# Performance work log

Measured on AMD Instinct MI355X. Metric: run time of the kernel, lower is better.

The kernel has to match this reference:

```python
import jax, jax.numpy as jnp
import numpy as np
from jax import lax

BIN_SIZE = 16.0
SIGMA = 2.0
THRESHOLD = 0.3
MIN_VOTES = 50.0
ACC = 24  # static accumulator extent per dim; provably >= max bin span for these inputs
BIG = 1_000_000


def setup_inputs() -> dict:
    key = jax.random.key(0)
    k1, k2 = jax.random.split(key)
    offsets = jax.random.normal(k1, (4, 2, 256, 256), dtype=jnp.float32)
    foreground_mask = jax.random.randint(k2, (4, 256, 256), 0, 2).astype(bool)
    return {"offsets": offsets, "foreground_mask": foreground_mask}


def hough_labels(offsets, foreground_mask):
    B, S = offsets.shape[:2]
    H, W = offsets.shape[2:]
    N = H * W

    # coordinate grid: channel 0 = x (last spatial dim), channel 1 = y (reversed meshgrid)
    ys, xs = jnp.meshgrid(jnp.arange(H, dtype=jnp.float32),
                          jnp.arange(W, dtype=jnp.float32), indexing='ij')
    coords = jnp.stack([xs, ys], axis=0)                      # [2, H, W]

    votes = coords[None] + offsets                            # [B, 2, H, W]
    bins = jnp.round(votes / BIN_SIZE).astype(jnp.int32).reshape(B, S, N)  # [B, 2, N]
    fg = foreground_mask.reshape(B, N)                        # [B, N]

    # per-batch min bin over foreground pixels -> shift to non-negative indices
    bin_min = jnp.min(jnp.where(fg[:, None, :], bins, BIG), axis=2)        # [B, 2]
    shifted = bins - bin_min[:, :, None]                                   # [B, 2, N]
    bin_max = jnp.max(jnp.where(fg[:, None, :], shifted, -1), axis=2) + 1  # [B, 2]

    # scatter-add vote counts into a static [ACC, ACC] accumulator per batch
    s0 = jnp.clip(shifted[:, 0], 0, ACC - 1)
    s1 = jnp.clip(shifted[:, 1], 0, ACC - 1)
    w = fg.astype(jnp.float32)
    bidx = jnp.broadcast_to(jnp.arange(B)[:, None], (B, N))
    acc = jnp.zeros((B, ACC, ACC), jnp.float32).at[bidx, s0, s1].add(w)

    # mean-filter smoothing (k = int(3*sigma)*2+1), zero padding, same shape
    k = int(3 * SIGMA) * 2 + 1
    kernel = jnp.ones((1, 1, k, k), jnp.float32) / float(k * k)
    sm = lax.conv_general_dilated(acc[:, None], kernel, (1, 1),
                                  [(k // 2, k // 2)] * 2)[:, 0]            # [B, ACC, ACC]

    # zero out cells beyond the tight (data-dependent) torch accumulator extent
    i = jnp.arange(ACC)
    valid = (i[None, :, None] < bin_max[:, 0, None, None]) & \
            (i[None, None, :] < bin_max[:, 1, None, None])
    sm = jnp.where(valid, sm, 0.0)

    # peak detection: relative threshold vs min_votes floor
    thr = jnp.maximum(sm.max(axis=(1, 2)) * THRESHOLD, MIN_VOTES)          # [B]
    peaks = (sm >= thr[:, None, None]).reshape(B, ACC * ACC)               # [B, C]
    # 1-based row-major rank of each peak cell (matches torch.nonzero ordering)
    ranks = jnp.cumsum(peaks.astype(jnp.int32), axis=1)                    # [B, C]

    # nearest-peak assignment (squared L2 preserves cdist argmin)
    c0, c1 = jnp.meshgrid(i, i, indexing='ij')
    cells = jnp.stack([c0.ravel(), c1.ravel()], axis=-1).astype(jnp.float32)  # [C, 2]
    fb = shifted.transpose(0, 2, 1).astype(jnp.float32)                    # [B, N, 2]
    d2 = jnp.sum((fb[:, :, None, :] - cells[None, None]) ** 2, axis=-1)    # [B, N, C]
    d2 = jnp.where(peaks[:, None, :], d2, jnp.inf)
    nearest_cell = jnp.argmin(d2, axis=2)                                  # [B, N]
    labels = jnp.take_along_axis(ranks, nearest_cell, axis=1)              # [B, N]
    labels = jnp.where(fg, labels, 0)
    return labels.reshape(B, H, W)


def reference(offsets, foreground_mask):
    return hough_labels(offsets, foreground_mask)
```

## Files before the change

kernel.cpp:

```cpp
#include <hip/hip_runtime.h>

#define NB   4
#define NPIX 65536
#define ACCD 24
#define NC   576
#define HD   32
#define HC   1024
#define HOFF 8
#define BIGV 1000000
#define INFKEY 0x3FFFFFFF


__device__ __forceinline__ int2 bin_of(float ox, float oy, int x, int y) {
  return make_int2((int)rintf(((float)x + ox) * 0.0625f),
                   (int)rintf(((float)y + oy) * 0.0625f));
}

__global__ void __launch_bounds__(1024) k_hist(const float* __restrict__ off,
                                               const int* __restrict__ fg,
                                               unsigned* __restrict__ part) {
  const int tid = threadIdx.x;
  const int b = blockIdx.x >> 4;
  const int n0 = ((blockIdx.x & 15) << 12) | (tid << 2);

  __shared__ unsigned hist[HC];
  hist[tid] = 0u;
  __syncthreads();

  const float4 ox4 = *(const float4*)&off[(b * 2 + 0) * NPIX + n0];
  const float4 oy4 = *(const float4*)&off[(b * 2 + 1) * NPIX + n0];
  const int4 f4 = *(const int4*)&fg[b * NPIX + n0];
  const float oxs[4] = {ox4.x, ox4.y, ox4.z, ox4.w};
  const float oys[4] = {oy4.x, oy4.y, oy4.z, oy4.w};
  const int fgs[4] = {f4.x, f4.y, f4.z, f4.w};
#pragma unroll
  for (int u = 0; u < 4; ++u) {
    if (fgs[u] != 0) {
      const int n = n0 + u;
      const int2 bb = bin_of(oxs[u], oys[u], n & 255, n >> 8);
      const int h0 = min(max(bb.x + HOFF, 0), HD - 1);
      const int h1 = min(max(bb.y + HOFF, 0), HD - 1);
      atomicAdd(&hist[h0 * HD + h1], 1u);
    }
  }
  __syncthreads();
  part[blockIdx.x * HC + tid] = hist[tid];
}

__global__ void __launch_bounds__(1024) k_finish(const float* __restrict__ off,
                                                 const int* __restrict__ fg,
                                                 const unsigned* __restrict__ part,
                                                 int* __restrict__ out) {
  const int tid = threadIdx.x;
  const int lane = tid & 63, wid = tid >> 6;
  const int b = blockIdx.x >> 4;
  const int sl = blockIdx.x & 15;

  __shared__ int hist[HC];
  __shared__ int cnt[NC];
  __shared__ int rowsum[NC];
  __shared__ int cellrank[NC];
  __shared__ int gkey[NC];
  __shared__ int tbl[NC];
  __shared__ int wred[16][4];
  __shared__ float wmaxs[16];
  __shared__ unsigned long long masks[16];

  int v = 0;
#pragma unroll
  for (int k = 0; k < 16; ++k) v += (int)part[(b * 16 + k) * HC + tid];
  hist[tid] = v;

  {
    int rmn = v > 0 ? (tid >> 5) : BIGV, rmx = v > 0 ? (tid >> 5) : -BIGV;
    int cmn = v > 0 ? (tid & 31) : BIGV, cmx = v > 0 ? (tid & 31) : -BIGV;
    for (int o = 32; o > 0; o >>= 1) {
      rmn = min(rmn, __shfl_xor(rmn, o, 64));
      rmx = max(rmx, __shfl_xor(rmx, o, 64));
      cmn = min(cmn, __shfl_xor(cmn, o, 64));
      cmx = max(cmx, __shfl_xor(cmx, o, 64));
    }
    if (lane == 0) { wred[wid][0] = rmn; wred[wid][1] = rmx; wred[wid][2] = cmn; wred[wid][3] = cmx; }
  }
  __syncthreads();
  int rmin = BIGV, rmax = -BIGV, cmin = BIGV, cmax = -BIGV;
#pragma unroll
  for (int w = 0; w < 16; ++w) {
    rmin = min(rmin, wred[w][0]); rmax = max(rmax, wred[w][1]);
    cmin = min(cmin, wred[w][2]); cmax = max(cmax, wred[w][3]);
  }
  const int vm0 = rmax - rmin + 1, vm1 = cmax - cmin + 1;

  const bool act = tid < NC;
  const int ci = act ? tid / ACCD : 0, cj = act ? tid % ACCD : 0;
  if (act) {
    const int ri = rmin + ci, rj = cmin + cj;
    cnt[tid] = ((unsigned)ri < HD && (unsigned)rj < HD) ? hist[ri * HD + rj] : 0;
  }
  __syncthreads();

  if (act) {
    int s = 0;
    const int j0 = max(cj - 6, 0), j1 = min(cj + 6, ACCD - 1);
    for (int jj = j0; jj <= j1; ++jj) s += cnt[ci * ACCD + jj];
    rowsum[tid] = s;
  }
  __syncthreads();
  float sm = 0.f;
  if (act) {
    int sum = 0;
    const int i0 = max(ci - 6, 0), i1 = min(ci + 6, ACCD - 1);
    for (int ii = i0; ii <= i1; ++ii) sum += rowsum[ii * ACCD + cj];
    sm = (float)sum * (1.0f / 169.0f);
    if (ci >= vm0 || cj >= vm1) sm = 0.f;
  }

  {
    float m = sm;
    for (int o = 32; o > 0; o >>= 1) m = fmaxf(m, __shfl_xor(m, o, 64));
    if (lane == 0) wmaxs[wid] = m;
  }
  __syncthreads();
  float mm = wmaxs[0];
#pragma unroll
  for (int w = 1; w < 16; ++w) mm = fmaxf(mm, wmaxs[w]);
  const float thr = fmaxf(mm * 0.3f, 50.0f);

  const bool flag = act && (sm >= thr);
  const unsigned long long mask = __ballot(flag);
  if (lane == 0) masks[wid] = mask;
  __syncthreads();
  int pref = 0, P = 0;
#pragma unroll
  for (int w = 0; w < 16; ++w) {
    const int c = (int)__popcll(masks[w]);
    if (w < wid) pref += c;
    P += c;
  }
  if (act)
    cellrank[tid] = flag ? (pref + (int)__popcll(mask & ((1ull << lane) - 1ull)))
                         : INFKEY;
  __syncthreads();

  if (act) {
    int g = INFKEY;
#pragma unroll
    for (int ii = 0; ii < ACCD; ++ii) {
      const int d = ci - ii;
      g = min(g, (d * d << 10) + cellrank[ii * ACCD + cj]);
    }
    gkey[tid] = g;
  }
  __syncthreads();

  if (act) {
    int key = INFKEY;
#pragma unroll
    for (int jj = 0; jj < ACCD; ++jj) {
      const int d = cj - jj;
      key = min(key, (d * d << 10) + gkey[ci * ACCD + jj]);
    }
    tbl[tid] = (P > 0) ? ((key & 1023) + 1) : 0;
  }
  __syncthreads();

  const int n0 = (sl << 12) | (tid << 2);
  const float4 ox4 = *(const float4*)&off[(b * 2 + 0) * NPIX + n0];
  const float4 oy4 = *(const float4*)&off[(b * 2 + 1) * NPIX + n0];
  const int4 f4 = *(const int4*)&fg[b * NPIX + n0];
  const float oxs[4] = {ox4.x, ox4.y, ox4.z, ox4.w};
  const float oys[4] = {oy4.x, oy4.y, oy4.z, oy4.w};
  const int fgs[4] = {f4.x, f4.y, f4.z, f4.w};
  int lab[4];
#pragma unroll
  for (int u = 0; u < 4; ++u) {
    lab[u] = 0;
    if (fgs[u] != 0) {
      const int n = n0 + u;
      const int2 bb = bin_of(oxs[u], oys[u], n & 255, n >> 8);
      const int h0 = min(max(bb.x + HOFF, 0), HD - 1);
      const int h1 = min(max(bb.y + HOFF, 0), HD - 1);
      const int s0 = min(max(h0 - rmin, 0), ACCD - 1);
      const int s1 = min(max(h1 - cmin, 0), ACCD - 1);
      lab[u] = tbl[s0 * ACCD + s1];
    }
  }
  *(int4*)&out[b * NPIX + n0] = make_int4(lab[0], lab[1], lab[2], lab[3]);
}

extern "C" void kernel_launch(void* const* d_in, const int* in_sizes, int n_in,
                              void* d_out, int out_size, void* d_ws, size_t ws_size,
                              hipStream_t stream) {
  const float* off = (const float*)d_in[0];
  const int* fg = (const int*)d_in[1];
  int* out = (int*)d_out;
  unsigned* part = (unsigned*)d_ws;

  k_hist<<<64, 1024, 0, stream>>>(off, fg, part);
  k_finish<<<64, 1024, 0, stream>>>(off, fg, part, out);
}
```

Baseline: 18.07 us.

## Fuse histogram and labeling kernels using per-batch global atomic barrier

Merges the two kernels into one. Each block accumulates its local histogram into a global per-batch histogram with atomics, then spins on a per-batch counter until all 16 blocks of that batch arrive. Each pixel's bin is kept in a register, so offsets are read and binned only once instead of twice. It adds a memset launch and a spin-wait barrier, and relies on all 64 blocks being co-resident.

```diff
diff --git a/kernel.cpp b/kernel.cpp
--- a/kernel.cpp
+++ b/kernel.cpp
@@ -16,41 +16,11 @@
                    (int)rintf(((float)y + oy) * 0.0625f));
 }
 
-__global__ void __launch_bounds__(1024) k_hist(const float* __restrict__ off,
-                                               const int* __restrict__ fg,
-                                               unsigned* __restrict__ part) {
-  const int tid = threadIdx.x;
-  const int b = blockIdx.x >> 4;
-  const int n0 = ((blockIdx.x & 15) << 12) | (tid << 2);
-
-  __shared__ unsigned hist[HC];
-  hist[tid] = 0u;
-  __syncthreads();
-
-  const float4 ox4 = *(const float4*)&off[(b * 2 + 0) * NPIX + n0];
-  const float4 oy4 = *(const float4*)&off[(b * 2 + 1) * NPIX + n0];
-  const int4 f4 = *(const int4*)&fg[b * NPIX + n0];
-  const float oxs[4] = {ox4.x, ox4.y, ox4.z, ox4.w};
-  const float oys[4] = {oy4.x, oy4.y, oy4.z, oy4.w};
-  const int fgs[4] = {f4.x, f4.y, f4.z, f4.w};
-#pragma unroll
-  for (int u = 0; u < 4; ++u) {
-    if (fgs[u] != 0) {
-      const int n = n0 + u;
-      const int2 bb = bin_of(oxs[u], oys[u], n & 255, n >> 8);
-      const int h0 = min(max(bb.x + HOFF, 0), HD - 1);
-      const int h1 = min(max(bb.y + HOFF, 0), HD - 1);
-      atomicAdd(&hist[h0 * HD + h1], 1u);
-    }
-  }
-  __syncthreads();
-  part[blockIdx.x * HC + tid] = hist[tid];
-}
-
-__global__ void __launch_bounds__(1024) k_finish(const float* __restrict__ off,
-                                                 const int* __restrict__ fg,
-                                                 const unsigned* __restrict__ part,
-                                                 int* __restrict__ out) {
+__global__ void __launch_bounds__(1024) k_fused(const float* __restrict__ off,
+                                                const int* __restrict__ fg,
+                                                unsigned* __restrict__ ghist,
+                                                unsigned* __restrict__ ctr,
+                                                int* __restrict__ out) {
   const int tid = threadIdx.x;
   const int lane = tid & 63, wid = tid >> 6;
   const int b = blockIdx.x >> 4;
@@ -66,14 +36,48 @@
   __shared__ float wmaxs[16];
   __shared__ unsigned long long masks[16];
 
-  int v = 0;
+  hist[tid] = 0;
+  __syncthreads();
+
+  const int n0 = (sl << 12) | (tid << 2);
+  const float4 ox4 = *(const float4*)&off[(b * 2 + 0) * NPIX + n0];
+  const float4 oy4 = *(const float4*)&off[(b * 2 + 1) * NPIX + n0];
+  const int4 f4 = *(const int4*)&fg[b * NPIX + n0];
+  const float oxs[4] = {ox4.x, ox4.y, ox4.z, ox4.w};
+  const float oys[4] = {oy4.x, oy4.y, oy4.z, oy4.w};
+  const int fgs[4] = {f4.x, f4.y, f4.z, f4.w};
+  int mybin[4];
 #pragma unroll
-  for (int k = 0; k < 16; ++k) v += (int)part[(b * 16 + k) * HC + tid];
-  hist[tid] = v;
+  for (int u = 0; u < 4; ++u) {
+    const int n = n0 + u;
+    const int2 bb = bin_of(oxs[u], oys[u], n & 255, n >> 8);
+    const int h0 = min(max(bb.x + HOFF, 0), HD - 1);
+    const int h1 = min(max(bb.y + HOFF, 0), HD - 1);
+    mybin[u] = ((fgs[u] != 0) ? 0x8000 : 0) | (h0 << 5) | h1;
+    if (fgs[u] != 0) atomicAdd((unsigned*)&hist[h0 * HD + h1], 1u);
+  }
+  __syncthreads();
 
   {
-    int rmn = v > 0 ? (tid >> 5) : BIGV, rmx = v > 0 ? (tid >> 5) : -BIGV;
-    int cmn = v > 0 ? (tid & 31) : BIGV, cmx = v > 0 ? (tid & 31) : -BIGV;
+    const unsigned v = (unsigned)hist[tid];
+    if (v) atomicAdd(&ghist[b * HC + tid], v);
+  }
+  __threadfence();
+  __syncthreads();
+
+  if (tid == 0) {
+    __hip_atomic_fetch_add(&ctr[b], 1u, __ATOMIC_RELEASE, __HIP_MEMORY_SCOPE_AGENT);
+    while (__hip_atomic_load(&ctr[b], __ATOMIC_ACQUIRE, __HIP_MEMORY_SCOPE_AGENT) < 16u) {}
+  }
+  __syncthreads();
+
+  const int hv = (int)__hip_atomic_load(&ghist[b * HC + tid], __ATOMIC_RELAXED,
+                                        __HIP_MEMORY_SCOPE_AGENT);
+  hist[tid] = hv;
+
+  {
+    int rmn = hv > 0 ? (tid >> 5) : BIGV, rmx = hv > 0 ? (tid >> 5) : -BIGV;
+    int cmn = hv > 0 ? (tid & 31) : BIGV, cmx = hv > 0 ? (tid & 31) : -BIGV;
     for (int o = 32; o > 0; o >>= 1) {
       rmn = min(rmn, __shfl_xor(rmn, o, 64));
       rmx = max(rmx, __shfl_xor(rmx, o, 64));
@@ -121,10 +125,10 @@
     if (lane == 0) wmaxs[wid] = m;
   }
   __syncthreads();
-  float mm = wmaxs[0];
+  float mmx = wmaxs[0];
 #pragma unroll
-  for (int w = 1; w < 16; ++w) mm = fmaxf(mm, wmaxs[w]);
-  const float thr = fmaxf(mm * 0.3f, 50.0f);
+  for (int w = 1; w < 16; ++w) mmx = fmaxf(mmx, wmaxs[w]);
+  const float thr = fmaxf(mmx * 0.3f, 50.0f);
 
   const bool flag = act && (sm >= thr);
   const unsigned long long mask = __ballot(flag);
@@ -164,22 +168,12 @@
   }
   __syncthreads();
 
-  const int n0 = (sl << 12) | (tid << 2);
-  const float4 ox4 = *(const float4*)&off[(b * 2 + 0) * NPIX + n0];
-  const float4 oy4 = *(const float4*)&off[(b * 2 + 1) * NPIX + n0];
-  const int4 f4 = *(const int4*)&fg[b * NPIX + n0];
-  const float oxs[4] = {ox4.x, ox4.y, ox4.z, ox4.w};
-  const float oys[4] = {oy4.x, oy4.y, oy4.z, oy4.w};
-  const int fgs[4] = {f4.x, f4.y, f4.z, f4.w};
   int lab[4];
 #pragma unroll
   for (int u = 0; u < 4; ++u) {
     lab[u] = 0;
-    if (fgs[u] != 0) {
-      const int n = n0 + u;
-      const int2 bb = bin_of(oxs[u], oys[u], n & 255, n >> 8);
-      const int h0 = min(max(bb.x + HOFF, 0), HD - 1);
-      const int h1 = min(max(bb.y + HOFF, 0), HD - 1);
+    if (mybin[u] & 0x8000) {
+      const int h0 = (mybin[u] >> 5) & 31, h1 = mybin[u] & 31;
       const int s0 = min(max(h0 - rmin, 0), ACCD - 1);
       const int s1 = min(max(h1 - cmin, 0), ACCD - 1);
       lab[u] = tbl[s0 * ACCD + s1];
@@ -194,8 +188,9 @@
   const float* off = (const float*)d_in[0];
   const int* fg = (const int*)d_in[1];
   int* out = (int*)d_out;
-  unsigned* part = (unsigned*)d_ws;
+  unsigned* ghist = (unsigned*)d_ws;
+  unsigned* ctr = ghist + NB * HC;
 
-  k_hist<<<64, 1024, 0, stream>>>(off, fg, part);
-  k_finish<<<64, 1024, 0, stream>>>(off, fg, part, out);
+  hipMemsetAsync(d_ws, 0, (NB * HC + NB) * sizeof(unsigned), stream);
+  k_fused<<<64, 1024, 0, stream>>>(off, fg, ghist, ctr, out);
 }
```

New measurement: 35.32 us. 95.5% more time.
